# Performance work log

Measured on AMD Instinct MI355X. Metric: run time of the kernel, lower is better.

Reference implementation:

```python
import jax, jax.numpy as jnp
import numpy as np
import math

LOG2 = math.log(2.0)

def shifted_softplus(x):
    return jax.nn.softplus(x) - LOG2

def setup_inputs() -> dict:
    key = jax.random.key(0)
    ks = jax.random.split(key, 12)
    n_atoms, n_pairs = 40000, 640000
    d_basis, d_filt, n_rbf = 128, 128, 20
    x = jax.random.normal(ks[0], (n_atoms, d_basis), dtype=jnp.float32)
    f_ij = jax.random.uniform(ks[1], (n_pairs, n_rbf), dtype=jnp.float32)
    idx_i = jax.random.randint(ks[2], (n_pairs,), 0, n_atoms)
    idx_j = jax.random.randint(ks[3], (n_pairs,), 0, n_atoms)
    rcut_ij = jax.random.uniform(ks[4], (n_pairs,), dtype=jnp.float32)
    s_in = 1.0 / math.sqrt(d_basis)
    s_f = 1.0 / math.sqrt(n_rbf)
    s_out = 1.0 / math.sqrt(d_filt)
    W_in = jax.random.uniform(ks[5], (d_filt, d_basis), minval=-s_in, maxval=s_in)
    b_in = jax.random.uniform(ks[6], (d_filt,), minval=-s_in, maxval=s_in)
    W_f = jax.random.uniform(ks[7], (d_filt, n_rbf), minval=-s_f, maxval=s_f)
    b_f = jax.random.uniform(ks[8], (d_filt,), minval=-s_f, maxval=s_f)
    W_out = jax.random.uniform(ks[9], (d_basis, d_filt), minval=-s_out, maxval=s_out)
    b_out = jax.random.uniform(ks[10], (d_basis,), minval=-s_out, maxval=s_out)
    return {"x": x, "f_ij": f_ij, "idx_i": idx_i, "idx_j": idx_j, "rcut_ij": rcut_ij,
            "W_in": W_in, "b_in": b_in, "W_f": W_f, "b_f": b_f, "W_out": W_out, "b_out": b_out}

def reference(x, f_ij, idx_i, idx_j, rcut_ij, W_in, b_in, W_f, b_f, W_out, b_out):
    n_atoms = x.shape[0]
    # input_to_feature: Linear(d_basis -> d_filt)
    h = x @ W_in.T + b_in                                  # [n_atoms, d_filt]
    # filter_network: Linear(n_rbf -> d_filt) + ShiftedSoftplus, scaled by cutoff
    Wij = shifted_softplus(f_ij @ W_f.T + b_f) * rcut_ij[:, None]  # [n_pairs, d_filt]
    # gather neighbor features, modulate, scatter-add back to atoms
    x_ij = h[idx_j] * Wij                                  # [n_pairs, d_filt]
    agg = jax.ops.segment_sum(x_ij, idx_i, num_segments=n_atoms)   # [n_atoms, d_filt]
    # feature_to_output: Linear(d_filt -> d_basis) + ShiftedSoftplus
    return shifted_softplus(agg @ W_out.T + b_out)
```

## Files before the change

kernel.cpp:

```cpp
#include <hip/hip_runtime.h>
#include <hip/hip_bf16.h>
#include <hip/hip_fp16.h>

typedef __hip_bfloat16 bf16;
typedef __attribute__((ext_vector_type(8))) short short8;
typedef __attribute__((ext_vector_type(4))) float f32x4;

__device__ __forceinline__ float braw2f(unsigned short u) {
    return __uint_as_float(((unsigned int)u) << 16);
}
__device__ __forceinline__ unsigned short f2braw(float f) {
    bf16 b = __float2bfloat16(f);
    return *(unsigned short*)&b;
}
__device__ __forceinline__ unsigned int pack2(float lo, float hi) {
    return (unsigned int)f2braw(lo) | ((unsigned int)f2braw(hi) << 16);
}
__device__ __forceinline__ float h2f(unsigned short u) {
    __half h = *(__half*)&u;
    return __half2float(h);
}

#define LN2F 0.69314718055994531f
__device__ __forceinline__ float ssp(float x) {
    return fmaxf(x, 0.0f) + __logf(1.0f + __expf(-fabsf(x))) - LN2F;
}

template<bool ACT, bool OUT_BF16>
__global__ __launch_bounds__(256) void linear128_mfma_kernel(
    const float* __restrict__ X, const float* __restrict__ W, const float* __restrict__ Bias,
    void* __restrict__ Yv, int n_rows)
{
    __shared__ unsigned short wls[128 * 128];
    __shared__ unsigned short xs[64 * 128];
    __shared__ float bls[128];

    const float4* W4 = (const float4*)W;
    for (int i = threadIdx.x; i < 128 * 32; i += 256) {
        float4 w = W4[i];
        ushort4 s; s.x = f2braw(w.x); s.y = f2braw(w.y); s.z = f2braw(w.z); s.w = f2braw(w.w);
        *(ushort4*)&wls[i * 4] = s;
    }
    if (threadIdx.x < 128) bls[threadIdx.x] = Bias[threadIdx.x];

    const int base = blockIdx.x * 64;
    const float4* X4 = (const float4*)X;
    for (int i = threadIdx.x; i < 64 * 32; i += 256) {
        int r = i >> 5, k4 = i & 31;
        int row = base + r;
        float4 v = (row < n_rows) ? X4[(size_t)row * 32 + k4] : make_float4(0.f, 0.f, 0.f, 0.f);
        ushort4 s; s.x = f2braw(v.x); s.y = f2braw(v.y); s.z = f2braw(v.z); s.w = f2braw(v.w);
        *(ushort4*)&xs[r * 128 + k4 * 4] = s;
    }
    __syncthreads();

    const int wv = threadIdx.x >> 6;
    const int l  = threadIdx.x & 63;
    const int lm = l & 15;
    const int lq = l >> 4;

    short8 a[4];
    #pragma unroll
    for (int kk = 0; kk < 4; ++kk)
        a[kk] = *(const short8*)&xs[(wv * 16 + lm) * 128 + kk * 32 + lq * 8];

    f32x4 acc[8];
    #pragma unroll
    for (int ct = 0; ct < 8; ++ct) {
        f32x4 c = {0.f, 0.f, 0.f, 0.f};
        #pragma unroll
        for (int kk = 0; kk < 4; ++kk) {
            short8 b = *(const short8*)&wls[(ct * 16 + lm) * 128 + kk * 32 + lq * 8];
            c = __builtin_amdgcn_mfma_f32_16x16x32_bf16(a[kk], b, c, 0, 0, 0);
        }
        acc[ct] = c;
    }

    #pragma unroll
    for (int ct = 0; ct < 8; ++ct) {
        int col = ct * 16 + lm;
        float bia = bls[col];
        #pragma unroll
        for (int r = 0; r < 4; ++r) {
            int row = base + wv * 16 + lq * 4 + r;
            if (row < n_rows) {
                float o = acc[ct][r] + bia;
                if (ACT) o = ssp(o);
                if (OUT_BF16) ((unsigned short*)Yv)[(size_t)row * 128 + col] = f2braw(o);
                else          ((float*)Yv)[(size_t)row * 128 + col] = o;
            }
        }
    }
}


__global__ __launch_bounds__(256) void zero_int_kernel(int* __restrict__ p, int n) {
    int i = blockIdx.x * 256 + threadIdx.x;
    if (i < n) p[i] = 0;
}

__global__ __launch_bounds__(256) void zero2_kernel(
    int* __restrict__ a, int na, int* __restrict__ b, int nb)
{
    int i = blockIdx.x * 256 + threadIdx.x;
    if (i < na) a[i] = 0;
    int j = i - na;
    if (j >= 0 && j < nb) b[j] = 0;
}

__global__ __launch_bounds__(256) void hist_kernel(
    const int* __restrict__ idx_i, int* __restrict__ cnt, int n_pairs, int n_atoms)
{
    for (int p = blockIdx.x * 256 + threadIdx.x; p < n_pairs; p += gridDim.x * 256) {
        int ai = idx_i[p];
        if ((unsigned)ai < (unsigned)n_atoms) atomicAdd(&cnt[ai], 1);
    }
}

__global__ __launch_bounds__(1024) void scan1_kernel(
    const int* __restrict__ cnt, int* __restrict__ offs, int* __restrict__ partials, int n)
{
    __shared__ int sm[1024];
    int t = threadIdx.x, idx = blockIdx.x * 1024 + t;
    int v = (idx < n) ? cnt[idx] : 0;
    sm[t] = v;
    __syncthreads();
    #pragma unroll
    for (int d = 1; d < 1024; d <<= 1) {
        int tmp = (t >= d) ? sm[t - d] : 0;
        __syncthreads();
        sm[t] += tmp;
        __syncthreads();
    }
    if (idx < n) offs[idx] = sm[t] - v;
    if (t == 1023) partials[blockIdx.x] = sm[1023];
}

__global__ __launch_bounds__(64) void scan2_kernel(
    int* __restrict__ partials, int* __restrict__ offs, int nb, int n)
{
    __shared__ int sm[64];
    int t = threadIdx.x;
    int v = (t < nb) ? partials[t] : 0;
    sm[t] = v;
    __syncthreads();
    #pragma unroll
    for (int d = 1; d < 64; d <<= 1) {
        int tmp = (t >= d) ? sm[t - d] : 0;
        __syncthreads();
        sm[t] += tmp;
        __syncthreads();
    }
    if (t < nb) partials[t] = sm[t] - v;
    if (t == 63) offs[n] = sm[63];
}

__global__ __launch_bounds__(1024) void scan3_kernel(
    int* __restrict__ offs, int* __restrict__ cur, const int* __restrict__ partials, int n)
{
    int idx = blockIdx.x * 1024 + threadIdx.x;
    if (idx < n) {
        int o = offs[idx] + partials[blockIdx.x];
        offs[idx] = o;
        cur[idx] = o;
    }
}

template<bool WRITE_ATOM>
__global__ __launch_bounds__(256) void scatter_pay_kernel(
    const float* __restrict__ f_ij, const int* __restrict__ idx_i, const int* __restrict__ idx_j,
    const float* __restrict__ rcut, int* __restrict__ cur, uint4* __restrict__ pay,
    int* __restrict__ pair_atom, int n_pairs, int n_atoms)
{
    if (blockIdx.x == 0 && threadIdx.x < 204) {
        ((int*)(pay + (size_t)n_pairs * 3))[threadIdx.x] = 0;
    }
    for (int p = blockIdx.x * 256 + threadIdx.x; p < n_pairs; p += gridDim.x * 256) {
        int ai = idx_i[p];
        if ((unsigned)ai >= (unsigned)n_atoms) continue;
        int pos = atomicAdd(&cur[ai], 1);
        const float4* fr = (const float4*)(f_ij + (size_t)p * 20);
        float4 f0 = fr[0], f1 = fr[1], f2 = fr[2], f3 = fr[3], f4 = fr[4];
        uint4 q0, q1, q2;
        q0.x = pack2(f0.x, f0.y); q0.y = pack2(f0.z, f0.w);
        q0.z = pack2(f1.x, f1.y); q0.w = pack2(f1.z, f1.w);
        q1.x = pack2(f2.x, f2.y); q1.y = pack2(f2.z, f2.w);
        q1.z = pack2(f3.x, f3.y); q1.w = pack2(f3.z, f3.w);
        q2.x = pack2(f4.x, f4.y); q2.y = pack2(f4.z, f4.w);
        q2.z = (unsigned int)idx_j[p];
        q2.w = __float_as_uint(rcut[p]);
        uint4* dst = pay + (size_t)pos * 3;
        dst[0] = q0; dst[1] = q1; dst[2] = q2;
        if (WRITE_ATOM) pair_atom[pos] = ai;
    }
}

#define FP_NITER 4

__global__ __launch_bounds__(256) void fused_pair_kernel(
    const uint4* __restrict__ pay, const int* __restrict__ pair_atom,
    const float* __restrict__ W_f, const float* __restrict__ b_f,
    const unsigned int* __restrict__ hb32, float* __restrict__ agg, int n_pairs)
{
    __shared__ unsigned short wls[128 * 40];
    __shared__ float bls[128];
    __shared__ unsigned short wij[4][16 * 132];
    __shared__ int lds_atom[4][16];
    __shared__ int lds_aj[4][16];

    for (int i = threadIdx.x; i < 128 * 32; i += 256) {
        int col = i >> 5, k = i & 31;
        float v = (k < 20) ? W_f[col * 20 + k] : 0.f;
        wls[col * 40 + k] = f2braw(v);
    }
    if (threadIdx.x < 128) bls[threadIdx.x] = b_f[threadIdx.x];
    __syncthreads();

    const int wv = threadIdx.x >> 6;
    const int l  = threadIdx.x & 63;
    const int lm = l & 15;
    const int lq = l >> 4;

    const int base = (blockIdx.x * 4 + wv) * (16 * FP_NITER);
    float a0 = 0.f, a1 = 0.f;
    int cura = -1;

    for (int t = 0; t < FP_NITER; ++t) {
        const int p0 = base + t * 16;
        if (p0 >= n_pairs) break;

        if (l < 16) {
            int p = p0 + l;
            bool valid = p < n_pairs;
            lds_atom[wv][l] = valid ? pair_atom[p] : -1;
            lds_aj[wv][l]   = valid ? (int)((const unsigned int*)pay)[(size_t)p * 12 + 10] : 0;
        }

        const char* rec = (const char*)pay + (size_t)(p0 + lm) * 48;
        short8 a = *(const short8*)(rec + lq * 16);
        if (lq == 2) { a[4] = 0; a[5] = 0; a[6] = 0; a[7] = 0; }
        if (lq == 3) { a[0]=0; a[1]=0; a[2]=0; a[3]=0; a[4]=0; a[5]=0; a[6]=0; a[7]=0; }

        f32x4 acc[8];
        #pragma unroll
        for (int ct = 0; ct < 8; ++ct) {
            short8 b = *(const short8*)&wls[(ct * 16 + lm) * 40 + lq * 8];
            f32x4 z = {0.f, 0.f, 0.f, 0.f};
            acc[ct] = __builtin_amdgcn_mfma_f32_16x16x32_bf16(a, b, z, 0, 0, 0);
        }

        float rc[4];
        #pragma unroll
        for (int r = 0; r < 4; ++r) {
            int p = p0 + lq * 4 + r;
            rc[r] = (p < n_pairs) ? ((const float*)pay)[(size_t)p * 12 + 11] : 0.f;
        }
        #pragma unroll
        for (int ct = 0; ct < 8; ++ct) {
            float bia = bls[ct * 16 + lm];
            #pragma unroll
            for (int r = 0; r < 4; ++r) {
                float o = ssp(acc[ct][r] + bia) * rc[r];
                __half hh = __float2half(o);
                wij[wv][(lq * 4 + r) * 132 + ct * 16 + lm] = *(unsigned short*)&hh;
            }
        }

        asm volatile("s_waitcnt lgkmcnt(0)" ::: "memory");

        int nv = n_pairs - p0;
        if (nv > 16) nv = 16;
        #pragma unroll 4
        for (int k = 0; k < nv; ++k) {
            int pa = lds_atom[wv][k];
            if (pa != cura) {
                if (cura >= 0) {
                    atomicAdd(&agg[(size_t)cura * 128 + 2 * l], a0);
                    atomicAdd(&agg[(size_t)cura * 128 + 2 * l + 1], a1);
                }
                a0 = 0.f; a1 = 0.f; cura = pa;
            }
            int aj = lds_aj[wv][k];
            unsigned int h = hb32[(size_t)aj * 64 + l];
            unsigned int w = *(const unsigned int*)&wij[wv][k * 132 + 2 * l];
            a0 += __uint_as_float(h << 16) * h2f((unsigned short)(w & 0xffffu));
            a1 += __uint_as_float(h & 0xffff0000u) * h2f((unsigned short)(w >> 16));
        }
    }
    if (cura >= 0) {
        atomicAdd(&agg[(size_t)cura * 128 + 2 * l], a0);
        atomicAdd(&agg[(size_t)cura * 128 + 2 * l + 1], a1);
    }
}

__global__ __launch_bounds__(256) void segment_pay_kernel(
    const uint4* __restrict__ pay, const float* __restrict__ W_f,
    const float* __restrict__ b_f, const unsigned int* __restrict__ hb32,
    const int* __restrict__ offs, float* __restrict__ agg, int n_atoms)
{
    const int wave = (blockIdx.x * 256 + threadIdx.x) >> 6;
    const int lane = threadIdx.x & 63;
    if (wave >= n_atoms) return;

    const int c0 = 2 * lane;
    float w0[20], w1[20];
    #pragma unroll
    for (int r = 0; r < 20; ++r) {
        w0[r] = W_f[c0 * 20 + r];
        w1[r] = W_f[(c0 + 1) * 20 + r];
    }
    const float b0 = b_f[c0], b1 = b_f[c0 + 1];

    const int cs = offs[wave], ce = offs[wave + 1];
    float acc0 = 0.f, acc1 = 0.f;

    int s = cs;
    for (; s + 2 <= ce; s += 2) {
        const uint4* pA = pay + (size_t)s * 3;
        const uint4* pB = pA + 3;
        uint4 qA0 = pA[0], qA1 = pA[1], qA2 = pA[2];
        uint4 qB0 = pB[0], qB1 = pB[1], qB2 = pB[2];
        unsigned int uA[10] = {qA0.x,qA0.y,qA0.z,qA0.w,qA1.x,qA1.y,qA1.z,qA1.w,qA2.x,qA2.y};
        unsigned int uB[10] = {qB0.x,qB0.y,qB0.z,qB0.w,qB1.x,qB1.y,qB1.z,qB1.w,qB2.x,qB2.y};
        float a0A = b0, a1A = b1, a0B = b0, a1B = b1;
        #pragma unroll
        for (int r = 0; r < 10; ++r) {
            float loA = __uint_as_float(uA[r] << 16);
            float hiA = __uint_as_float(uA[r] & 0xffff0000u);
            float loB = __uint_as_float(uB[r] << 16);
            float hiB = __uint_as_float(uB[r] & 0xffff0000u);
            a0A += loA * w0[2*r];     a1A += loA * w1[2*r];
            a0A += hiA * w0[2*r + 1]; a1A += hiA * w1[2*r + 1];
            a0B += loB * w0[2*r];     a1B += loB * w1[2*r];
            a0B += hiB * w0[2*r + 1]; a1B += hiB * w1[2*r + 1];
        }
        float rcA = __uint_as_float(qA2.w), rcB = __uint_as_float(qB2.w);
        float wv0A = ssp(a0A) * rcA, wv1A = ssp(a1A) * rcA;
        float wv0B = ssp(a0B) * rcB, wv1B = ssp(a1B) * rcB;
        unsigned int hA = hb32[(size_t)(int)qA2.z * 64 + lane];
        unsigned int hB = hb32[(size_t)(int)qB2.z * 64 + lane];
        acc0 += __uint_as_float(hA << 16) * wv0A + __uint_as_float(hB << 16) * wv0B;
        acc1 += __uint_as_float(hA & 0xffff0000u) * wv1A + __uint_as_float(hB & 0xffff0000u) * wv1B;
    }
    if (s < ce) {
        const uint4* pA = pay + (size_t)s * 3;
        uint4 q0 = pA[0], q1 = pA[1], q2 = pA[2];
        unsigned int u[10] = {q0.x,q0.y,q0.z,q0.w,q1.x,q1.y,q1.z,q1.w,q2.x,q2.y};
        float a0 = b0, a1 = b1;
        #pragma unroll
        for (int r = 0; r < 10; ++r) {
            float lo = __uint_as_float(u[r] << 16);
            float hi = __uint_as_float(u[r] & 0xffff0000u);
            a0 += lo * w0[2*r];     a1 += lo * w1[2*r];
            a0 += hi * w0[2*r + 1]; a1 += hi * w1[2*r + 1];
        }
        float rc = __uint_as_float(q2.w);
        float wv0 = ssp(a0) * rc, wv1 = ssp(a1) * rc;
        unsigned int h = hb32[(size_t)(int)q2.z * 64 + lane];
        acc0 += __uint_as_float(h << 16) * wv0;
        acc1 += __uint_as_float(h & 0xffff0000u) * wv1;
    }

    *(float2*)&agg[(size_t)wave * 128 + c0] = make_float2(acc0, acc1);
}

__global__ __launch_bounds__(256) void scatter_kernel(
    const int* __restrict__ idx_i, int* __restrict__ cur, int* __restrict__ perm,
    int n_pairs, int n_atoms)
{
    for (int p = blockIdx.x * 256 + threadIdx.x; p < n_pairs; p += gridDim.x * 256) {
        int ai = idx_i[p];
        if ((unsigned)ai < (unsigned)n_atoms) {
            int pos = atomicAdd(&cur[ai], 1);
            perm[pos] = p;
        }
    }
}

__global__ __launch_bounds__(256) void segment_kernel(
    const float* __restrict__ f_ij, const int* __restrict__ idx_j,
    const float* __restrict__ rcut, const float* __restrict__ W_f,
    const float* __restrict__ b_f, const unsigned short* __restrict__ hb,
    const int* __restrict__ offs, const int* __restrict__ perm,
    float* __restrict__ agg, int n_atoms)
{
    const int wave = (blockIdx.x * 256 + threadIdx.x) >> 6;
    const int lane = threadIdx.x & 63;
    if (wave >= n_atoms) return;

    float w0[20], w1[20];
    #pragma unroll
    for (int r = 0; r < 20; ++r) {
        w0[r] = W_f[lane * 20 + r];
        w1[r] = W_f[(lane + 64) * 20 + r];
    }
    const float b0 = b_f[lane], b1 = b_f[lane + 64];

    const int cs = offs[wave], ce = offs[wave + 1];
    float acc0 = 0.f, acc1 = 0.f;

    int s = cs;
    for (; s + 2 <= ce; s += 2) {
        int pA = perm[s], pB = perm[s + 1];
        int ajA = idx_j[pA], ajB = idx_j[pB];
        float rcA = rcut[pA], rcB = rcut[pB];
        const float4* frA = (const float4*)(f_ij + (size_t)pA * 20);
        const float4* frB = (const float4*)(f_ij + (size_t)pB * 20);
        float a0A = b0, a1A = b1, a0B = b0, a1B = b1;
        #pragma unroll
        for (int q = 0; q < 5; ++q) {
            float4 fA = frA[q], fB = frB[q];
            a0A += fA.x * w0[4*q+0]; a1A += fA.x * w1[4*q+0];
            a0A += fA.y * w0[4*q+1]; a1A += fA.y * w1[4*q+1];
            a0A += fA.z * w0[4*q+2]; a1A += fA.z * w1[4*q+2];
            a0A += fA.w * w0[4*q+3]; a1A += fA.w * w1[4*q+3];
            a0B += fB.x * w0[4*q+0]; a1B += fB.x * w1[4*q+0];
            a0B += fB.y * w0[4*q+1]; a1B += fB.y * w1[4*q+1];
            a0B += fB.z * w0[4*q+2]; a1B += fB.z * w1[4*q+2];
            a0B += fB.w * w0[4*q+3]; a1B += fB.w * w1[4*q+3];
        }
        float wv0A = ssp(a0A) * rcA, wv1A = ssp(a1A) * rcA;
        float wv0B = ssp(a0B) * rcB, wv1B = ssp(a1B) * rcB;
        float h0A = braw2f(hb[(size_t)ajA * 128 + lane]);
        float h1A = braw2f(hb[(size_t)ajA * 128 + 64 + lane]);
        float h0B = braw2f(hb[(size_t)ajB * 128 + lane]);
        float h1B = braw2f(hb[(size_t)ajB * 128 + 64 + lane]);
        acc0 += h0A * wv0A + h0B * wv0B;
        acc1 += h1A * wv1A + h1B * wv1B;
    }
    if (s < ce) {
        int p = perm[s];
        int aj = idx_j[p];
        float rc = rcut[p];
        const float4* fr = (const float4*)(f_ij + (size_t)p * 20);
        float a0 = b0, a1 = b1;
        #pragma unroll
        for (int q = 0; q < 5; ++q) {
            float4 fv = fr[q];
            a0 += fv.x * w0[4*q+0]; a1 += fv.x * w1[4*q+0];
            a0 += fv.y * w0[4*q+1]; a1 += fv.y * w1[4*q+1];
            a0 += fv.z * w0[4*q+2]; a1 += fv.z * w1[4*q+2];
            a0 += fv.w * w0[4*q+3]; a1 += fv.w * w1[4*q+3];
        }
        float wv0 = ssp(a0) * rc, wv1 = ssp(a1) * rc;
        acc0 += braw2f(hb[(size_t)aj * 128 + lane]) * wv0;
        acc1 += braw2f(hb[(size_t)aj * 128 + 64 + lane]) * wv1;
    }

    agg[(size_t)wave * 128 + lane]      = acc0;
    agg[(size_t)wave * 128 + 64 + lane] = acc1;
}

static inline size_t align_up(size_t v, size_t a) { return (v + a - 1) & ~(a - 1); }

extern "C" void kernel_launch(void* const* d_in, const int* in_sizes, int n_in,
                              void* d_out, int out_size, void* d_ws, size_t ws_size,
                              hipStream_t stream) {
    const float* x     = (const float*)d_in[0];
    const float* f_ij  = (const float*)d_in[1];
    const int*   idx_i = (const int*)d_in[2];
    const int*   idx_j = (const int*)d_in[3];
    const float* rcut  = (const float*)d_in[4];
    const float* W_in  = (const float*)d_in[5];
    const float* b_in  = (const float*)d_in[6];
    const float* W_f   = (const float*)d_in[7];
    const float* b_f   = (const float*)d_in[8];
    const float* W_out = (const float*)d_in[9];
    const float* b_out = (const float*)d_in[10];

    const int n_atoms = in_sizes[0] / 128;
    const int n_pairs = in_sizes[2];
    const int nscan = (n_atoms + 1023) / 1024;
    const int mfma_grid = (n_atoms + 63) / 64;

    size_t off_hb   = 0;
    size_t off_offs = align_up(off_hb + (size_t)n_atoms * 128 * 2, 16);
    size_t off_cur  = align_up(off_offs + (size_t)(n_atoms + 1) * 4, 16);
    size_t off_part = align_up(off_cur + (size_t)n_atoms * 4, 16);
    size_t off_pay  = align_up(off_part + (size_t)nscan * 4, 64);
    size_t need_pay = off_pay + (size_t)n_pairs * 48;
    size_t off_pa   = align_up(off_pay + (size_t)n_pairs * 48 + 816, 256);
    size_t need_fused = off_pa + (size_t)(n_pairs + 64) * 4;

    if (ws_size >= need_fused) {
        unsigned short* hb  = (unsigned short*)((char*)d_ws + off_hb);
        int*   offs = (int*)((char*)d_ws + off_offs);
        int*   cur  = (int*)((char*)d_ws + off_cur);
        int*   part = (int*)((char*)d_ws + off_part);
        uint4* pay  = (uint4*)((char*)d_ws + off_pay);
        int*   pair_atom = (int*)((char*)d_ws + off_pa);
        float* agg = (float*)d_out;

        linear128_mfma_kernel<false, true><<<dim3(mfma_grid), dim3(256), 0, stream>>>(
            x, W_in, b_in, (void*)hb, n_atoms);

        zero2_kernel<<<dim3((n_atoms * 128 + n_atoms + 255) / 256), dim3(256), 0, stream>>>(
            (int*)agg, n_atoms * 128, cur, n_atoms);

        hist_kernel<<<dim3(1024), dim3(256), 0, stream>>>(idx_i, cur, n_pairs, n_atoms);
        scan1_kernel<<<dim3(nscan), dim3(1024), 0, stream>>>(cur, offs, part, n_atoms);
        scan2_kernel<<<dim3(1), dim3(64), 0, stream>>>(part, offs, nscan, n_atoms);
        scan3_kernel<<<dim3(nscan), dim3(1024), 0, stream>>>(offs, cur, part, n_atoms);
        scatter_pay_kernel<true><<<dim3(1024), dim3(256), 0, stream>>>(
            f_ij, idx_i, idx_j, rcut, cur, pay, pair_atom, n_pairs, n_atoms);

        int fp_blocks = (n_pairs + 64 * FP_NITER - 1) / (64 * FP_NITER);
        fused_pair_kernel<<<dim3(fp_blocks), dim3(256), 0, stream>>>(
            pay, pair_atom, W_f, b_f, (const unsigned int*)hb, agg, n_pairs);

        linear128_mfma_kernel<true, false><<<dim3(mfma_grid), dim3(256), 0, stream>>>(
            agg, W_out, b_out, d_out, n_atoms);
    } else if (ws_size >= need_pay) {
        unsigned short* hb = (unsigned short*)((char*)d_ws + off_hb);
        int*  offs = (int*)((char*)d_ws + off_offs);
        int*  cur  = (int*)((char*)d_ws + off_cur);
        int*  part = (int*)((char*)d_ws + off_part);
        uint4* pay = (uint4*)((char*)d_ws + off_pay);
        float* agg = (float*)d_out;

        linear128_mfma_kernel<false, true><<<dim3(mfma_grid), dim3(256), 0, stream>>>(
            x, W_in, b_in, (void*)hb, n_atoms);

        zero_int_kernel<<<dim3((n_atoms + 255) / 256), dim3(256), 0, stream>>>(cur, n_atoms);
        hist_kernel<<<dim3(1024), dim3(256), 0, stream>>>(idx_i, cur, n_pairs, n_atoms);
        scan1_kernel<<<dim3(nscan), dim3(1024), 0, stream>>>(cur, offs, part, n_atoms);
        scan2_kernel<<<dim3(1), dim3(64), 0, stream>>>(part, offs, nscan, n_atoms);
        scan3_kernel<<<dim3(nscan), dim3(1024), 0, stream>>>(offs, cur, part, n_atoms);
        scatter_pay_kernel<false><<<dim3(1024), dim3(256), 0, stream>>>(
            f_ij, idx_i, idx_j, rcut, cur, pay, (int*)nullptr, n_pairs, n_atoms);

        segment_pay_kernel<<<dim3((n_atoms + 3) / 4), dim3(256), 0, stream>>>(
            pay, W_f, b_f, (const unsigned int*)hb, offs, agg, n_atoms);

        linear128_mfma_kernel<true, false><<<dim3(mfma_grid), dim3(256), 0, stream>>>(
            agg, W_out, b_out, d_out, n_atoms);
    } else {
        size_t o_h    = 0;
        size_t o_offs = o_h + (size_t)n_atoms * 128 * 2;
        size_t o_cur  = o_offs + (size_t)(n_atoms + 1) * 4;
        size_t o_perm = o_cur + (size_t)n_atoms * 4;
        size_t o_part = o_perm + (size_t)n_pairs * 4;
        unsigned short* hb = (unsigned short*)((char*)d_ws + o_h);
        int* offs = (int*)((char*)d_ws + o_offs);
        int* cur  = (int*)((char*)d_ws + o_cur);
        int* perm = (int*)((char*)d_ws + o_perm);
        int* part = (int*)((char*)d_ws + o_part);
        float* agg = (float*)d_out;

        linear128_mfma_kernel<false, true><<<dim3(mfma_grid), dim3(256), 0, stream>>>(
            x, W_in, b_in, (void*)hb, n_atoms);

        zero_int_kernel<<<dim3((n_atoms + 255) / 256), dim3(256), 0, stream>>>(cur, n_atoms);
        hist_kernel<<<dim3(1024), dim3(256), 0, stream>>>(idx_i, cur, n_pairs, n_atoms);
        scan1_kernel<<<dim3(nscan), dim3(1024), 0, stream>>>(cur, offs, part, n_atoms);
        scan2_kernel<<<dim3(1), dim3(64), 0, stream>>>(part, offs, nscan, n_atoms);
        scan3_kernel<<<dim3(nscan), dim3(1024), 0, stream>>>(offs, cur, part, n_atoms);
        scatter_kernel<<<dim3(1024), dim3(256), 0, stream>>>(idx_i, cur, perm, n_pairs, n_atoms);

        segment_kernel<<<dim3((n_atoms + 3) / 4), dim3(256), 0, stream>>>(
            f_ij, idx_j, rcut, W_f, b_f, hb, offs, perm, agg, n_atoms);

        linear128_mfma_kernel<true, false><<<dim3(mfma_grid), dim3(256), 0, stream>>>(
            agg, W_out, b_out, d_out, n_atoms);
    }
}
```

Before: 368.6 us.

## Prefetch neighbor gathers into registers and keep filter weights in registers

The fused pair kernel now issues the 16 per-tile gathers of h[idx_j] and the pair_atom loads into registers before the MFMA and softplus stage, so gather latency can overlap the filter computation. The W_f fragments and bias now live in per-lane registers instead of being staged through LDS, which removes the block-wide preamble and __syncthreads. Atom ids are made wave-uniform with readfirstlane, and launch bounds request 4 blocks per CU. The risk is register pressure: hreg and pa are indexed by a runtime-bounded, partially unrolled loop, which may force them into scratch memory.

```diff
diff --git a/kernel.cpp b/kernel.cpp
--- a/kernel.cpp
+++ b/kernel.cpp
@@ -197,30 +197,35 @@
 
 #define FP_NITER 4
 
-__global__ __launch_bounds__(256) void fused_pair_kernel(
+__global__ __launch_bounds__(256, 4) void fused_pair_kernel(
     const uint4* __restrict__ pay, const int* __restrict__ pair_atom,
     const float* __restrict__ W_f, const float* __restrict__ b_f,
     const unsigned int* __restrict__ hb32, float* __restrict__ agg, int n_pairs)
 {
-    __shared__ unsigned short wls[128 * 40];
-    __shared__ float bls[128];
     __shared__ unsigned short wij[4][16 * 132];
-    __shared__ int lds_atom[4][16];
-    __shared__ int lds_aj[4][16];
-
-    for (int i = threadIdx.x; i < 128 * 32; i += 256) {
-        int col = i >> 5, k = i & 31;
-        float v = (k < 20) ? W_f[col * 20 + k] : 0.f;
-        wls[col * 40 + k] = f2braw(v);
-    }
-    if (threadIdx.x < 128) bls[threadIdx.x] = b_f[threadIdx.x];
-    __syncthreads();
 
     const int wv = threadIdx.x >> 6;
     const int l  = threadIdx.x & 63;
     const int lm = l & 15;
     const int lq = l >> 4;
 
+    short8 bfrag[8];
+    float bias[8];
+    #pragma unroll
+    for (int ct = 0; ct < 8; ++ct) {
+        const int col = ct * 16 + lm;
+        short8 b;
+        #pragma unroll
+        for (int e = 0; e < 8; ++e) {
+            int k = lq * 8 + e;
+            float v = (k < 20) ? W_f[col * 20 + k] : 0.f;
+            b[e] = (short)f2braw(v);
+        }
+        bfrag[ct] = b;
+        bias[ct] = b_f[col];
+    }
+
+    const unsigned int* payu = (const unsigned int*)pay;
     const int base = (blockIdx.x * 4 + wv) * (16 * FP_NITER);
     float a0 = 0.f, a1 = 0.f;
     int cura = -1;
@@ -228,12 +233,18 @@
     for (int t = 0; t < FP_NITER; ++t) {
         const int p0 = base + t * 16;
         if (p0 >= n_pairs) break;
-
-        if (l < 16) {
-            int p = p0 + l;
+        int nv = n_pairs - p0;
+        if (nv > 16) nv = 16;
+
+        int pa[16];
+        unsigned int hreg[16];
+        #pragma unroll
+        for (int k = 0; k < 16; ++k) {
+            int p = p0 + k;
             bool valid = p < n_pairs;
-            lds_atom[wv][l] = valid ? pair_atom[p] : -1;
-            lds_aj[wv][l]   = valid ? (int)((const unsigned int*)pay)[(size_t)p * 12 + 10] : 0;
+            pa[k] = __builtin_amdgcn_readfirstlane(valid ? pair_atom[p] : -1);
+            int ajk = valid ? (int)payu[(size_t)p * 12 + 10] : 0;
+            hreg[k] = hb32[(size_t)ajk * 64 + l];
         }
 
         const char* rec = (const char*)pay + (size_t)(p0 + lm) * 48;
@@ -241,26 +252,20 @@
         if (lq == 2) { a[4] = 0; a[5] = 0; a[6] = 0; a[7] = 0; }
         if (lq == 3) { a[0]=0; a[1]=0; a[2]=0; a[3]=0; a[4]=0; a[5]=0; a[6]=0; a[7]=0; }
 
-        f32x4 acc[8];
-        #pragma unroll
-        for (int ct = 0; ct < 8; ++ct) {
-            short8 b = *(const short8*)&wls[(ct * 16 + lm) * 40 + lq * 8];
-            f32x4 z = {0.f, 0.f, 0.f, 0.f};
-            acc[ct] = __builtin_amdgcn_mfma_f32_16x16x32_bf16(a, b, z, 0, 0, 0);
-        }
-
         float rc[4];
         #pragma unroll
         for (int r = 0; r < 4; ++r) {
             int p = p0 + lq * 4 + r;
             rc[r] = (p < n_pairs) ? ((const float*)pay)[(size_t)p * 12 + 11] : 0.f;
         }
+
         #pragma unroll
         for (int ct = 0; ct < 8; ++ct) {
-            float bia = bls[ct * 16 + lm];
+            f32x4 z = {0.f, 0.f, 0.f, 0.f};
+            f32x4 acc = __builtin_amdgcn_mfma_f32_16x16x32_bf16(a, bfrag[ct], z, 0, 0, 0);
             #pragma unroll
             for (int r = 0; r < 4; ++r) {
-                float o = ssp(acc[ct][r] + bia) * rc[r];
+                float o = ssp(acc[r] + bias[ct]) * rc[r];
                 __half hh = __float2half(o);
                 wij[wv][(lq * 4 + r) * 132 + ct * 16 + lm] = *(unsigned short*)&hh;
             }
@@ -268,20 +273,17 @@
 
         asm volatile("s_waitcnt lgkmcnt(0)" ::: "memory");
 
-        int nv = n_pairs - p0;
-        if (nv > 16) nv = 16;
         #pragma unroll 4
         for (int k = 0; k < nv; ++k) {
-            int pa = lds_atom[wv][k];
-            if (pa != cura) {
+            int p_a = pa[k];
+            if (p_a != cura) {
                 if (cura >= 0) {
                     atomicAdd(&agg[(size_t)cura * 128 + 2 * l], a0);
                     atomicAdd(&agg[(size_t)cura * 128 + 2 * l + 1], a1);
                 }
-                a0 = 0.f; a1 = 0.f; cura = pa;
+                a0 = 0.f; a1 = 0.f; cura = p_a;
             }
-            int aj = lds_aj[wv][k];
-            unsigned int h = hb32[(size_t)aj * 64 + l];
+            unsigned int h = hreg[k];
             unsigned int w = *(const unsigned int*)&wij[wv][k * 132 + 2 * l];
             a0 += __uint_as_float(h << 16) * h2f((unsigned short)(w & 0xffffu));
             a1 += __uint_as_float(h & 0xffff0000u) * h2f((unsigned short)(w >> 16));
```

New measurement: 434.6 us. +17.9%, slower.
